# Kernel optimization log

Measured on AMD Instinct MI355X. Metric: run time of the kernel, lower is better.

## Reference

```python
import jax, jax.numpy as jnp
import numpy as np

N = 20000      # base graph nodes
S = 20         # nodes per subgraph
NC = N * S     # combined subgraph nodes = 400000
EC = 2_000_000 # combined subgraph edges
EB = 200_000   # base graph edges
NIN = 64
HOP = 16
D = NIN + HOP  # 80, conv width
NOUT = 64


def setup_inputs() -> dict:
    key = jax.random.key(0)
    ks = jax.random.split(key, 32)
    f32 = jnp.float32

    batch = jnp.repeat(jnp.arange(N), S)                      # subgraph id per combined node
    offs = jax.random.randint(ks[0], (NC,), 1, N)
    nodes_mapper = (batch + offs) % N                         # never equals batch
    cent_idx = jnp.arange(N) * S
    nodes_mapper = nodes_mapper.at[cent_idx].set(jnp.arange(N))  # exactly one centroid/subgraph

    edge_index = jax.random.randint(ks[1], (2, EC), 0, NC)
    edges_mapper = jax.random.randint(ks[2], (EC,), 0, EB)
    hop_indicator = jax.random.randint(ks[3], (NC,), 0, 19)   # +1 -> [1,19] < 20

    x = jax.random.normal(ks[4], (N, NIN), f32)
    edge_attr = jax.random.normal(ks[5], (EB, D), f32)

    def lin(k, i, o, s=0.05):
        return jax.random.normal(k, (i, o), f32) * s

    inp = dict(
        x=x, edge_attr=edge_attr,
        hop_table=jax.random.normal(ks[6], (20, HOP), f32) * 0.05,
        conv_w1=lin(ks[7], D, D), bn1_g=jnp.ones((D,), f32), bn1_b=jnp.zeros((D,), f32),
        conv_w2=lin(ks[8], D, D), bn2_g=jnp.ones((D,), f32), bn2_b=jnp.zeros((D,), f32),
        oe_w=lin(ks[9], D, NOUT), oe_b=jnp.zeros((NOUT,), f32),
        sub_w=lin(ks[10], NOUT, NOUT), sub_b=jnp.zeros((NOUT,), f32),
        sub_g=jnp.ones((NOUT,), f32), sub_bt=jnp.zeros((NOUT,), f32),
        ctx_w=lin(ks[11], NOUT, NOUT), ctx_b=jnp.zeros((NOUT,), f32),
        ctx_g=jnp.ones((NOUT,), f32), ctx_bt=jnp.zeros((NOUT,), f32),
        gc_w=lin(ks[12], HOP, NOUT), gc_b=jnp.zeros((NOUT,), f32),
        gs_w=lin(ks[13], HOP, NOUT), gs_b=jnp.zeros((NOUT,), f32),
        gx_w=lin(ks[14], HOP, NOUT), gx_b=jnp.zeros((NOUT,), f32),
        fo_w=lin(ks[15], NOUT, NOUT), fo_b=jnp.zeros((NOUT,), f32),
        fo_g=jnp.ones((NOUT,), f32), fo_bt=jnp.zeros((NOUT,), f32),
        nodes_mapper=nodes_mapper, edges_mapper=edges_mapper,
        edge_index=edge_index, batch=batch, hop_indicator=hop_indicator,
    )
    return inp


def reference(x, edge_attr, hop_table,
              conv_w1, bn1_g, bn1_b, conv_w2, bn2_g, bn2_b, oe_w, oe_b,
              sub_w, sub_b, sub_g, sub_bt, ctx_w, ctx_b, ctx_g, ctx_bt,
              gc_w, gc_b, gs_w, gs_b, gx_w, gx_b,
              fo_w, fo_b, fo_g, fo_bt,
              nodes_mapper, edges_mapper, edge_index, batch, hop_indicator):
    hop_emb = hop_table[hop_indicator + 1]                       # [NC, HOP]
    h = jnp.concatenate([x[nodes_mapper], hop_emb], axis=-1)     # [NC, D] gather + concat
    ea = edge_attr[edges_mapper]                                 # [EC, D] gather
    src, dst = edge_index[0], edge_index[1]

    def gine_layer(h, W, g, b):
        # GINEConv (eps=0, no bias): Linear(x_i + sum_j ReLU(x_j + e_ji)), then eval-BN + ReLU
        msg = jax.nn.relu(h[src] + ea)                           # [EC, D]
        agg = jax.ops.segment_sum(msg, dst, num_segments=NC)     # scatter-add
        out = (h + agg) @ W
        return jax.nn.relu(g * out + b)

    prev = h
    h = gine_layer(h, conv_w1, bn1_g, bn1_b) + prev
    prev = h
    h = gine_layer(h, conv_w2, bn2_g, bn2_b) + prev
    comb = h @ oe_w + oe_b                                       # [NC, NOUT] output encoder

    gate_c = jax.nn.sigmoid(hop_emb @ gc_w + gc_b)
    gate_s = jax.nn.sigmoid(hop_emb @ gs_w + gs_b)
    gate_x = jax.nn.sigmoid(hop_emb @ gx_w + gx_b)

    # centroid: exactly one node per subgraph with mapper==batch -> masked segment_sum picks it
    mask = (nodes_mapper == batch).astype(comb.dtype)[:, None]
    centroid = jax.ops.segment_sum(comb * gate_c * mask, batch, num_segments=N)

    sub = jax.nn.relu(sub_g * (comb @ sub_w + sub_b) + sub_bt) * gate_s
    ctx = jax.nn.relu(ctx_g * (comb @ ctx_w + ctx_b) + ctx_bt) * gate_x

    ones = jnp.ones((NC,), comb.dtype)
    cnt_b = jnp.clip(jax.ops.segment_sum(ones, batch, num_segments=N), 1.0)
    cnt_m = jnp.clip(jax.ops.segment_sum(ones, nodes_mapper, num_segments=N), 1.0)
    sub_pool = jax.ops.segment_sum(sub, batch, num_segments=N) / cnt_b[:, None]
    ctx_pool = jax.ops.segment_sum(ctx, nodes_mapper, num_segments=N) / cnt_m[:, None]

    out = centroid + sub_pool + ctx_pool                         # embs_combine_mode='add'
    return fo_g * (out @ fo_w + fo_b) + fo_bt                    # out_encoder: Linear + eval-BN
```

## Files before the change

kernel.cpp:

```cpp
#include <hip/hip_runtime.h>
#include <hip/hip_bf16.h>

#define N_    20000
#define S_    20
#define NC_   400000
#define EC_   2000000
#define EB_   200000
#define NIN_  64
#define HOP_  16
#define D_    80
#define NOUT_ 64
#define NB_   1563
#define NBN_  79

typedef __attribute__((ext_vector_type(8))) short bf16x8;
typedef __attribute__((ext_vector_type(4))) float f32x4;
union FragU { uint4 u; bf16x8 b; };

__device__ __forceinline__ float2 bf2f(unsigned u) {
    float2 r;
    r.x = __uint_as_float(u << 16);
    r.y = __uint_as_float(u & 0xffff0000u);
    return r;
}
__device__ __forceinline__ unsigned f2bf_rne(float f) {
    unsigned u = __float_as_uint(f);
    return (u + 0x7fffu + ((u >> 16) & 1u)) >> 16;
}
__device__ __forceinline__ unsigned pack2(float a, float b) {
    return f2bf_rne(a) | (f2bf_rne(b) << 16);
}
__device__ __forceinline__ unsigned addpk(unsigned a, unsigned b) {
    float2 fa = bf2f(a), fb = bf2f(b);
    return pack2(fa.x + fb.x, fa.y + fb.y);
}
__device__ __forceinline__ uint4 addpk4(uint4 A, uint4 B) {
    return make_uint4(addpk(A.x, B.x), addpk(A.y, B.y), addpk(A.z, B.z), addpk(A.w, B.w));
}

__device__ __forceinline__ int blockExclScan(int v, int tid, int* lds, int* total) {
    int lane = tid & 63;
    int w = tid >> 6;
    int x = v;
    #pragma unroll
    for (int off = 1; off < 64; off <<= 1) {
        int y = __shfl_up(x, off, 64);
        if (lane >= off) x += y;
    }
    if (lane == 63) lds[w] = x;
    __syncthreads();
    if (tid == 0) {
        int acc = 0;
        #pragma unroll
        for (int i = 0; i < 4; i++) { int t = lds[i]; lds[4 + i] = acc; acc += t; }
        lds[8] = acc;
    }
    __syncthreads();
    int res = x - v + lds[4 + w];
    *total = lds[8];
    return res;
}

__global__ __launch_bounds__(256) void k_degree(const int* __restrict__ eidx, int* __restrict__ deg) {
    int e = blockIdx.x * 256 + threadIdx.x;
    if (e >= EC_) return;
    atomicAdd(&deg[eidx[EC_ + e]], 1);
}

__global__ __launch_bounds__(256) void k_hist(const int* __restrict__ mapper, int* __restrict__ cnt) {
    int i = blockIdx.x * 256 + threadIdx.x;
    if (i >= NC_) return;
    atomicAdd(&cnt[mapper[i]], 1);
}

__global__ __launch_bounds__(256) void k_bsum(const int* __restrict__ deg, int* __restrict__ bsums, int n) {
    __shared__ int lds[9];
    int i = blockIdx.x * 256 + threadIdx.x;
    int v = (i < n) ? deg[i] : 0;
    int tot;
    blockExclScan(v, threadIdx.x, lds, &tot);
    if (threadIdx.x == 0) bsums[blockIdx.x] = tot;
}

__global__ __launch_bounds__(256) void k_scan_bsums(int* __restrict__ bsums, int nb) {
    __shared__ int lds[9];
    int carry = 0;
    for (int base = 0; base < nb; base += 256) {
        int i = base + threadIdx.x;
        int v = (i < nb) ? bsums[i] : 0;
        int tot;
        int ex = blockExclScan(v, threadIdx.x, lds, &tot);
        if (i < nb) bsums[i] = ex + carry;
        carry += tot;
        __syncthreads();
    }
}

__global__ __launch_bounds__(256) void k_scan_apply(
    int* __restrict__ cursor, int* __restrict__ start, const int* __restrict__ bsums,
    int n, int total)
{
    __shared__ int lds[9];
    int i = blockIdx.x * 256 + threadIdx.x;
    int v = (i < n) ? cursor[i] : 0;
    int tot;
    int ex = blockExclScan(v, threadIdx.x, lds, &tot);
    if (i < n) {
        int s = ex + bsums[blockIdx.x];
        start[i] = s;
        cursor[i] = s;
    }
    if (blockIdx.x == 0 && threadIdx.x == 0) start[n] = total;
}

__global__ __launch_bounds__(256) void k_fill(
    const int* __restrict__ eidx, const int* __restrict__ emap,
    const int* __restrict__ hop,
    int* __restrict__ cursor, int2* __restrict__ e2)
{
    int e = blockIdx.x * 256 + threadIdx.x;
    if (e >= EC_) return;
    int src = eidx[e];
    int dst = eidx[EC_ + e];
    int pk = emap[e] * 32 + (hop[src] + 1);
    int pos = atomicAdd(&cursor[dst], 1);
    e2[pos] = make_int2(src, pk);
}

__global__ __launch_bounds__(256) void k_fill_nodes(
    const int* __restrict__ mapper, int* __restrict__ cursor, int* __restrict__ nidx)
{
    int i = blockIdx.x * 256 + threadIdx.x;
    if (i >= NC_) return;
    int pos = atomicAdd(&cursor[mapper[i]], 1);
    nidx[pos] = i;
}

__global__ __launch_bounds__(256) void k_xb16(unsigned* __restrict__ xb, const float* __restrict__ x) {
    int idx = blockIdx.x * 256 + threadIdx.x;
    if (idx >= N_ * 32) return;
    int row = idx >> 5, p = idx & 31;
    float2 v = *(const float2*)(x + (size_t)row * 64 + 2 * p);
    xb[idx] = pack2(v.x, v.y);
}
__global__ __launch_bounds__(160) void k_htb16(unsigned* __restrict__ htb, const float* __restrict__ ht) {
    int idx = threadIdx.x;
    int row = idx >> 3, p = idx & 7;
    float2 v = *(const float2*)(ht + (size_t)row * 16 + 2 * p);
    htb[idx] = pack2(v.x, v.y);
}

__global__ __launch_bounds__(256) void k_ea16(
    unsigned* __restrict__ eab, const float* __restrict__ ea)
{
    int idx = blockIdx.x * 256 + threadIdx.x;
    if (idx >= EB_ * 40) return;
    int row = idx / 40, t = idx - row * 40;
    float2 v = *(const float2*)(ea + (size_t)row * 80 + 2 * t);
    eab[idx] = pack2(v.x, v.y);
}

__global__ __launch_bounds__(64) void k_gates(
    const float* __restrict__ ht,
    const float* __restrict__ gc_w, const float* __restrict__ gc_b,
    const float* __restrict__ gs_w, const float* __restrict__ gs_b,
    const float* __restrict__ gx_w, const float* __restrict__ gx_b,
    float* __restrict__ gall)
{
    int h = blockIdx.x;
    int d = threadIdx.x;
    const float* htr = ht + h * 16;
    float a = gc_b[d], b = gs_b[d], c = gx_b[d];
    #pragma unroll
    for (int k = 0; k < 16; k++) {
        float hk = htr[k];
        a += hk * gc_w[k * 64 + d];
        b += hk * gs_w[k * 64 + d];
        c += hk * gx_w[k * 64 + d];
    }
    gall[h * 64 + d]            = 1.f / (1.f + __expf(-a));
    gall[(20 + h) * 64 + d]     = 1.f / (1.f + __expf(-b));
    gall[(40 + h) * 64 + d]     = 1.f / (1.f + __expf(-c));
}

template<int L, bool EA16>
__global__ __launch_bounds__(320) void k_agg(
    const unsigned* __restrict__ hin, const unsigned* __restrict__ xb,
    const unsigned* __restrict__ htb, const int* __restrict__ mapper,
    const unsigned* __restrict__ eab, const float* __restrict__ eaf,
    const int* __restrict__ start, const int2* __restrict__ e2,
    unsigned* __restrict__ agg)
{
    int tid = threadIdx.x;
    int grp = tid / 40;
    int p = tid - grp * 40;
    int node = blockIdx.x * 8 + grp;
    float ax = 0.f, ay = 0.f;
    int e = start[node], s1 = start[node + 1];

    auto hload = [&](int src, int pk) -> float2 {
        if (L == 1) {
            if (p < 32) {
                int xs = mapper[src];
                return bf2f(xb[(size_t)xs * 32 + p]);
            } else {
                return bf2f(htb[(pk & 31) * 8 + (p - 32)]);
            }
        } else {
            return bf2f(hin[(size_t)src * 40 + p]);
        }
    };
    auto eload = [&](int pk) -> float2 {
        int em = pk >> 5;
        if (EA16) return bf2f(eab[(size_t)em * 40 + p]);
        else      return *(const float2*)(eaf + (size_t)em * 80 + 2 * p);
    };

    for (; e + 4 <= s1; e += 4) {
        int2 d0 = e2[e], d1 = e2[e + 1], d2 = e2[e + 2], d3 = e2[e + 3];
        float2 h0 = hload(d0.x, d0.y), h1 = hload(d1.x, d1.y);
        float2 h2 = hload(d2.x, d2.y), h3 = hload(d3.x, d3.y);
        float2 q0 = eload(d0.y), q1 = eload(d1.y), q2 = eload(d2.y), q3 = eload(d3.y);
        ax += fmaxf(h0.x + q0.x, 0.f) + fmaxf(h1.x + q1.x, 0.f)
            + fmaxf(h2.x + q2.x, 0.f) + fmaxf(h3.x + q3.x, 0.f);
        ay += fmaxf(h0.y + q0.y, 0.f) + fmaxf(h1.y + q1.y, 0.f)
            + fmaxf(h2.y + q2.y, 0.f) + fmaxf(h3.y + q3.y, 0.f);
    }
    for (; e < s1; e++) {
        int2 d0 = e2[e];
        float2 h0 = hload(d0.x, d0.y);
        float2 q0 = eload(d0.y);
        ax += fmaxf(h0.x + q0.x, 0.f);
        ay += fmaxf(h0.y + q0.y, 0.f);
    }
    agg[(size_t)node * 40 + p] = pack2(ax, ay);
}

template<int L>
__global__ __launch_bounds__(256) void k_lin(
    const unsigned* __restrict__ hbase, const unsigned* __restrict__ agg,
    unsigned* __restrict__ outp,
    const unsigned* __restrict__ xb, const unsigned* __restrict__ htb,
    const int* __restrict__ mapper, const int* __restrict__ hop,
    const float* __restrict__ W, const float* __restrict__ gv, const float* __restrict__ bv)
{
    __shared__ unsigned sWB[5 * 16 * 49];
    int tid = threadIdx.x;
    for (int i = tid; i < 5 * 16 * 49; i += 256) {
        int t = i / 784, r2 = i % 784, cc = r2 / 49, kp = r2 % 49;
        int col = 16 * t + cc;
        sWB[i] = (kp < 40) ? pack2(W[(2 * kp) * D_ + col], W[(2 * kp + 1) * D_ + col]) : 0u;
    }
    __syncthreads();

    int w = tid >> 6;
    int lane = tid & 63;
    int q = lane >> 4;
    int c = lane & 15;
    int base = (blockIdx.x * 4 + w) * 16;

    const unsigned* ar = agg + (size_t)(base + c) * 40;
    uint4 g0 = *(const uint4*)(ar + 4 * q);
    uint4 g1 = *(const uint4*)(ar + 16 + 4 * q);
    uint4 g2 = (q < 2) ? *(const uint4*)(ar + 32 + 4 * q) : make_uint4(0u, 0u, 0u, 0u);
    uint4 h0v, h1v, h2v;
    if (L == 1) {
        int m = mapper[base + c];
        int hp = hop[base + c] + 1;
        const unsigned* xr = xb + (size_t)m * 32;
        h0v = *(const uint4*)(xr + 4 * q);
        h1v = *(const uint4*)(xr + 16 + 4 * q);
        h2v = (q < 2) ? *(const uint4*)(htb + hp * 8 + 4 * q) : make_uint4(0u, 0u, 0u, 0u);
    } else {
        const unsigned* hr = hbase + (size_t)(base + c) * 40;
        h0v = *(const uint4*)(hr + 4 * q);
        h1v = *(const uint4*)(hr + 16 + 4 * q);
        h2v = (q < 2) ? *(const uint4*)(hr + 32 + 4 * q) : make_uint4(0u, 0u, 0u, 0u);
    }
    FragU a0, a1, a2;
    a0.u = addpk4(h0v, g0);
    a1.u = addpk4(h1v, g1);
    a2.u = (q < 2) ? addpk4(h2v, g2) : make_uint4(0u, 0u, 0u, 0u);

    f32x4 acc[5];
    #pragma unroll
    for (int t = 0; t < 5; t++) {
        const unsigned* pb = sWB + (t * 16 + c) * 49 + 4 * q;
        FragU b0, b1, b2;
        b0.u = *(const uint4*)(pb);
        b1.u = *(const uint4*)(pb + 16);
        b2.u = *(const uint4*)(pb + 32);
        f32x4 z = {0.f, 0.f, 0.f, 0.f};
        acc[t] = __builtin_amdgcn_mfma_f32_16x16x32_bf16(a0.b, b0.b, z, 0, 0, 0);
        acc[t] = __builtin_amdgcn_mfma_f32_16x16x32_bf16(a1.b, b1.b, acc[t], 0, 0, 0);
        acc[t] = __builtin_amdgcn_mfma_f32_16x16x32_bf16(a2.b, b2.b, acc[t], 0, 0, 0);
    }

    int mm2[4], hp2[4];
    if (L == 1) {
        #pragma unroll
        for (int r = 0; r < 4; r++) {
            int row = base + 4 * q + r;
            mm2[r] = mapper[row];
            hp2[r] = hop[row] + 1;
        }
    }
    #pragma unroll
    for (int t = 0; t < 5; t++) {
        int col = 16 * t + c;
        float gc_ = gv[col], bc_ = bv[col];
        #pragma unroll
        for (int r = 0; r < 4; r++) {
            int row = base + 4 * q + r;
            unsigned hu;
            if (L == 1) {
                hu = (t < 4) ? xb[(size_t)mm2[r] * 32 + 8 * t + (c >> 1)]
                             : htb[hp2[r] * 8 + (c >> 1)];
            } else {
                hu = hbase[(size_t)row * 40 + 8 * t + (c >> 1)];
            }
            float2 hf = bf2f(hu);
            float hres = (c & 1) ? hf.y : hf.x;
            float o = fmaxf(gc_ * acc[t][r] + bc_, 0.f) + hres;
            float partner = __shfl_xor(o, 1);
            if (!(c & 1)) outp[(size_t)row * 40 + 8 * t + (c >> 1)] = pack2(o, partner);
        }
    }
}

__global__ __launch_bounds__(256) void k_headm(
    const unsigned* __restrict__ h2u, const int* __restrict__ hop,
    const int* __restrict__ mapper, const float* __restrict__ gall,
    const float* __restrict__ oe_w, const float* __restrict__ oe_b,
    const float* __restrict__ sub_w, const float* __restrict__ sub_b,
    const float* __restrict__ sub_g, const float* __restrict__ sub_bt,
    const float* __restrict__ ctx_w, const float* __restrict__ ctx_b,
    const float* __restrict__ ctx_g, const float* __restrict__ ctx_bt,
    float* __restrict__ cent, float* __restrict__ subp, unsigned* __restrict__ ctxv)
{
    __shared__ unsigned sOE[4 * 16 * 48];
    __shared__ unsigned sSB[4 * 16 * 40];
    __shared__ unsigned sCX[4 * 16 * 40];
    __shared__ float    sT[4][16 * 68];
    int tid = threadIdx.x;
    for (int i = tid; i < 4 * 16 * 48; i += 256) {
        int t = i / (16 * 48), r2 = i % (16 * 48), cc = r2 / 48, kp = r2 % 48;
        int col = 16 * t + cc;
        sOE[i] = (kp < 40) ? pack2(oe_w[(2 * kp) * 64 + col], oe_w[(2 * kp + 1) * 64 + col]) : 0u;
    }
    for (int i = tid; i < 4 * 16 * 40; i += 256) {
        int t = i / (16 * 40), r2 = i % (16 * 40), cc = r2 / 40, kp = r2 % 40;
        int col = 16 * t + cc;
        bool ok = kp < 32;
        sSB[i] = ok ? pack2(sub_w[(2 * kp) * 64 + col], sub_w[(2 * kp + 1) * 64 + col]) : 0u;
        sCX[i] = ok ? pack2(ctx_w[(2 * kp) * 64 + col], ctx_w[(2 * kp + 1) * 64 + col]) : 0u;
    }
    __syncthreads();

    int w = tid >> 6;
    int lane = tid & 63;
    int q = lane >> 4;
    int c = lane & 15;
    int base = (blockIdx.x * 4 + w) * 16;

    const uint4* hrow = (const uint4*)(h2u + (size_t)(base + c) * 40);
    FragU a0, a1, a2;
    a0.u = hrow[q];
    a1.u = hrow[4 + q];
    a2.u = make_uint4(0u, 0u, 0u, 0u);
    if (q < 2) a2.u = hrow[8 + q];

    f32x4 acc[4];
    #pragma unroll
    for (int t = 0; t < 4; t++) {
        const unsigned* pb = sOE + (t * 16 + c) * 48 + 4 * q;
        FragU b0, b1, b2;
        b0.u = *(const uint4*)(pb);
        b1.u = *(const uint4*)(pb + 16);
        b2.u = *(const uint4*)(pb + 32);
        f32x4 z = {0.f, 0.f, 0.f, 0.f};
        acc[t] = __builtin_amdgcn_mfma_f32_16x16x32_bf16(a0.b, b0.b, z, 0, 0, 0);
        acc[t] = __builtin_amdgcn_mfma_f32_16x16x32_bf16(a1.b, b1.b, acc[t], 0, 0, 0);
        acc[t] = __builtin_amdgcn_mfma_f32_16x16x32_bf16(a2.b, b2.b, acc[t], 0, 0, 0);
    }

    int mm[4], hn[4];
    #pragma unroll
    for (int r = 0; r < 4; r++) {
        int node = base + 4 * q + r;
        mm[r] = mapper[node];
        hn[r] = hop[node] + 1;
    }
    int sgA = base / S_;
    int k0 = (sgA + 1) * S_ - base;
    if (k0 > 16) k0 = 16;

    #pragma unroll
    for (int t = 0; t < 4; t++) {
        int col = 16 * t + c;
        float ob = oe_b[col];
        #pragma unroll
        for (int r = 0; r < 4; r++) {
            int row = 4 * q + r;
            float v = acc[t][r] + ob;
            sT[w][row * 68 + col] = v;
            int sg = (row < k0) ? sgA : sgA + 1;
            if (mm[r] == sg) {
                cent[(size_t)sg * 64 + col] = v * gall[hn[r] * 64 + col];
            }
        }
    }

    const float* trp = &sT[w][c * 68 + 8 * q];
    float4 v0 = *(const float4*)(trp);
    float4 v1 = *(const float4*)(trp + 4);
    float4 v2 = *(const float4*)(trp + 32);
    float4 v3 = *(const float4*)(trp + 36);
    FragU ap0, ap1;
    ap0.u = make_uint4(pack2(v0.x, v0.y), pack2(v0.z, v0.w), pack2(v1.x, v1.y), pack2(v1.z, v1.w));
    ap1.u = make_uint4(pack2(v2.x, v2.y), pack2(v2.z, v2.w), pack2(v3.x, v3.y), pack2(v3.z, v3.w));

    f32x4 sa[4], ca[4];
    #pragma unroll
    for (int t = 0; t < 4; t++) {
        const unsigned* ps = sSB + (t * 16 + c) * 40 + 4 * q;
        const unsigned* pc = sCX + (t * 16 + c) * 40 + 4 * q;
        FragU b0, b1, d0, d1;
        b0.u = *(const uint4*)(ps);
        b1.u = *(const uint4*)(ps + 16);
        d0.u = *(const uint4*)(pc);
        d1.u = *(const uint4*)(pc + 16);
        f32x4 z = {0.f, 0.f, 0.f, 0.f};
        sa[t] = __builtin_amdgcn_mfma_f32_16x16x32_bf16(ap0.b, b0.b, z, 0, 0, 0);
        sa[t] = __builtin_amdgcn_mfma_f32_16x16x32_bf16(ap1.b, b1.b, sa[t], 0, 0, 0);
        ca[t] = __builtin_amdgcn_mfma_f32_16x16x32_bf16(ap0.b, d0.b, z, 0, 0, 0);
        ca[t] = __builtin_amdgcn_mfma_f32_16x16x32_bf16(ap1.b, d1.b, ca[t], 0, 0, 0);
    }

    #pragma unroll
    for (int t = 0; t < 4; t++) {
        int col = 16 * t + c;
        float sb = sub_b[col], sgm = sub_g[col], sbt = sub_bt[col];
        float cb = ctx_b[col], cgm = ctx_g[col], cbt = ctx_bt[col];
        float sA = 0.f, sB = 0.f;
        #pragma unroll
        for (int r = 0; r < 4; r++) {
            int row = 4 * q + r;
            float sval = fmaxf(sgm * (sa[t][r] + sb) + sbt, 0.f) * gall[(20 + hn[r]) * 64 + col];
            float cval = fmaxf(cgm * (ca[t][r] + cb) + cbt, 0.f) * gall[(40 + hn[r]) * 64 + col];
            float partner = __shfl_xor(cval, 1);
            if ((c & 1) == 0) {
                ctxv[(size_t)(base + row) * 32 + (col >> 1)] = pack2(cval, partner);
            }
            if (row < k0) sA += sval; else sB += sval;
        }
        sA += __shfl_xor(sA, 16); sA += __shfl_xor(sA, 32);
        sB += __shfl_xor(sB, 16); sB += __shfl_xor(sB, 32);
        if (q == 0) {
            atomicAdd(&subp[(size_t)sgA * 64 + col], sA);
            if (k0 < 16) atomicAdd(&subp[(size_t)(sgA + 1) * 64 + col], sB);
        }
    }
}

__global__ __launch_bounds__(256) void k_ctxpool(
    const unsigned* __restrict__ ctxv, const int* __restrict__ nstart,
    const int* __restrict__ nidx, float* __restrict__ ctxp)
{
    int w = threadIdx.x >> 6, d = threadIdx.x & 63;
    int n = blockIdx.x * 4 + w;
    if (n >= N_) return;
    int s0 = nstart[n], s1 = nstart[n + 1];
    int dh = d >> 1;
    float acc = 0.f;
    int i = s0;
    for (; i + 4 <= s1; i += 4) {
        int r0 = nidx[i], r1 = nidx[i + 1], r2 = nidx[i + 2], r3 = nidx[i + 3];
        float2 f0 = bf2f(ctxv[(size_t)r0 * 32 + dh]);
        float2 f1 = bf2f(ctxv[(size_t)r1 * 32 + dh]);
        float2 f2 = bf2f(ctxv[(size_t)r2 * 32 + dh]);
        float2 f3 = bf2f(ctxv[(size_t)r3 * 32 + dh]);
        acc += (d & 1) ? (f0.y + f1.y + f2.y + f3.y) : (f0.x + f1.x + f2.x + f3.x);
    }
    for (; i < s1; i++) {
        float2 f = bf2f(ctxv[(size_t)nidx[i] * 32 + dh]);
        acc += (d & 1) ? f.y : f.x;
    }
    ctxp[(size_t)n * 64 + d] = acc;
}

__global__ __launch_bounds__(256) void k_final(
    const float* __restrict__ cent, const float* __restrict__ subp, const float* __restrict__ ctxp,
    const int* __restrict__ nstart,
    const float* __restrict__ fo_w, const float* __restrict__ fo_b,
    const float* __restrict__ fo_g, const float* __restrict__ fo_bt,
    float* __restrict__ out)
{
    __shared__ float sW[64 * 64];
    int tid = threadIdx.x;
    for (int i = tid; i < 4096; i += 256) sW[i] = fo_w[i];
    int d = tid & 63, grp = tid >> 6;
    float rb = fo_b[d], rg = fo_g[d], rbt = fo_bt[d];
    __syncthreads();
    for (int n = blockIdx.x * 4 + grp; n < N_; n += gridDim.x * 4) {
        float cm = (float)max(nstart[n + 1] - nstart[n], 1);
        size_t o = (size_t)n * 64 + d;
        float r = cent[o] + subp[o] * (1.f / 20.f) + ctxp[o] / cm;
        float dot = rb;
        #pragma unroll 8
        for (int k = 0; k < 64; k++) dot += __shfl(r, k) * sW[k * 64 + d];
        out[o] = rg * dot + rbt;
    }
}

extern "C" void kernel_launch(void* const* d_in, const int* in_sizes, int n_in,
                              void* d_out, int out_size, void* d_ws, size_t ws_size,
                              hipStream_t stream) {
    const float* x         = (const float*)d_in[0];
    const float* edge_attr = (const float*)d_in[1];
    const float* hop_table = (const float*)d_in[2];
    const float* conv_w1   = (const float*)d_in[3];
    const float* bn1_g     = (const float*)d_in[4];
    const float* bn1_b     = (const float*)d_in[5];
    const float* conv_w2   = (const float*)d_in[6];
    const float* bn2_g     = (const float*)d_in[7];
    const float* bn2_b     = (const float*)d_in[8];
    const float* oe_w      = (const float*)d_in[9];
    const float* oe_b      = (const float*)d_in[10];
    const float* sub_w     = (const float*)d_in[11];
    const float* sub_b     = (const float*)d_in[12];
    const float* sub_g     = (const float*)d_in[13];
    const float* sub_bt    = (const float*)d_in[14];
    const float* ctx_w     = (const float*)d_in[15];
    const float* ctx_b     = (const float*)d_in[16];
    const float* ctx_g     = (const float*)d_in[17];
    const float* ctx_bt    = (const float*)d_in[18];
    const float* gc_w      = (const float*)d_in[19];
    const float* gc_b      = (const float*)d_in[20];
    const float* gs_w      = (const float*)d_in[21];
    const float* gs_b      = (const float*)d_in[22];
    const float* gx_w      = (const float*)d_in[23];
    const float* gx_b      = (const float*)d_in[24];
    const float* fo_w      = (const float*)d_in[25];
    const float* fo_b      = (const float*)d_in[26];
    const float* fo_g      = (const float*)d_in[27];
    const float* fo_bt     = (const float*)d_in[28];
    const int* nodes_mapper  = (const int*)d_in[29];
    const int* edges_mapper  = (const int*)d_in[30];
    const int* edge_index    = (const int*)d_in[31];
    const int* batch         = (const int*)d_in[32];
    const int* hop_indicator = (const int*)d_in[33];
    (void)batch;
    float* out = (float*)d_out;

    size_t off = 0;
    auto alloc = [&](size_t bytes) -> char* {
        char* p = (char*)d_ws + off;
        off = (off + bytes + 255) & ~(size_t)255;
        return p;
    };
    unsigned* hbuf0 = (unsigned*)alloc((size_t)NC_ * 40 * 4);
    unsigned* hbuf1 = (unsigned*)alloc((size_t)NC_ * 40 * 4);
    int*   start    = (int*)alloc((size_t)(NC_ + 1) * 4);
    int*   cursor   = (int*)alloc((size_t)NC_ * 4);
    int*   bsums    = (int*)alloc(2048 * 4);
    int2*  e2       = (int2*)alloc((size_t)EC_ * 8);
    float* cent     = (float*)alloc((size_t)N_ * 64 * 4);
    float* subp     = (float*)alloc((size_t)N_ * 64 * 4);
    float* ctxp     = (float*)alloc((size_t)N_ * 64 * 4);
    int*   nstart   = (int*)alloc((size_t)(N_ + 1) * 4);
    int*   cursor_n = (int*)alloc((size_t)N_ * 4);
    int*   bsums_n  = (int*)alloc(256 * 4);
    int*   nidx     = (int*)alloc((size_t)NC_ * 4);
    float* gall     = (float*)alloc((size_t)60 * 64 * 4);
    unsigned* xb    = (unsigned*)alloc((size_t)N_ * 32 * 4);
    unsigned* htb   = (unsigned*)alloc((size_t)20 * 8 * 4);
    size_t ea16_bytes = (size_t)EB_ * 40 * 4;
    bool use_ea16 = (off + ea16_bytes + 256) <= ws_size;
    unsigned* eab = use_ea16 ? (unsigned*)alloc(ea16_bytes) : nullptr;
    unsigned* ctxv = hbuf1;
    (void)in_sizes; (void)n_in; (void)out_size;

    hipMemsetAsync(cursor, 0, (size_t)NC_ * 4, stream);
    hipMemsetAsync(cursor_n, 0, (size_t)N_ * 4, stream);
    hipMemsetAsync(subp, 0, (size_t)N_ * 64 * 4, stream);

    k_xb16<<<(N_ * 32 + 255) / 256, 256, 0, stream>>>(xb, x);
    k_htb16<<<1, 160, 0, stream>>>(htb, hop_table);
    k_gates<<<20, 64, 0, stream>>>(hop_table, gc_w, gc_b, gs_w, gs_b, gx_w, gx_b, gall);
    if (use_ea16)
        k_ea16<<<(EB_ * 40 + 255) / 256, 256, 0, stream>>>(eab, edge_attr);

    k_degree<<<(EC_ + 255) / 256, 256, 0, stream>>>(edge_index, cursor);
    k_bsum<<<NB_, 256, 0, stream>>>(cursor, bsums, NC_);
    k_scan_bsums<<<1, 256, 0, stream>>>(bsums, NB_);
    k_scan_apply<<<NB_, 256, 0, stream>>>(cursor, start, bsums, NC_, EC_);
    k_fill<<<(EC_ + 255) / 256, 256, 0, stream>>>(edge_index, edges_mapper, hop_indicator,
                                                  cursor, e2);

    k_hist<<<(NC_ + 255) / 256, 256, 0, stream>>>(nodes_mapper, cursor_n);
    k_bsum<<<NBN_, 256, 0, stream>>>(cursor_n, bsums_n, N_);
    k_scan_bsums<<<1, 256, 0, stream>>>(bsums_n, NBN_);
    k_scan_apply<<<NBN_, 256, 0, stream>>>(cursor_n, nstart, bsums_n, N_, NC_);
    k_fill_nodes<<<(NC_ + 255) / 256, 256, 0, stream>>>(nodes_mapper, cursor_n, nidx);

    if (use_ea16)
        k_agg<1, true><<<NC_ / 8, 320, 0, stream>>>(nullptr, xb, htb, nodes_mapper,
                                                    eab, edge_attr, start, e2, hbuf0);
    else
        k_agg<1, false><<<NC_ / 8, 320, 0, stream>>>(nullptr, xb, htb, nodes_mapper,
                                                     eab, edge_attr, start, e2, hbuf0);
    k_lin<1><<<NC_ / 64, 256, 0, stream>>>(nullptr, hbuf0, hbuf1, xb, htb,
                                           nodes_mapper, hop_indicator,
                                           conv_w1, bn1_g, bn1_b);

    if (use_ea16)
        k_agg<2, true><<<NC_ / 8, 320, 0, stream>>>(hbuf1, xb, htb, nodes_mapper,
                                                    eab, edge_attr, start, e2, hbuf0);
    else
        k_agg<2, false><<<NC_ / 8, 320, 0, stream>>>(hbuf1, xb, htb, nodes_mapper,
                                                     eab, edge_attr, start, e2, hbuf0);
    k_lin<2><<<NC_ / 64, 256, 0, stream>>>(hbuf1, hbuf0, hbuf0, xb, htb,
                                           nodes_mapper, hop_indicator,
                                           conv_w2, bn2_g, bn2_b);

    k_headm<<<NC_ / 64, 256, 0, stream>>>(hbuf0, hop_indicator, nodes_mapper, gall,
                                          oe_w, oe_b, sub_w, sub_b, sub_g, sub_bt,
                                          ctx_w, ctx_b, ctx_g, ctx_bt,
                                          cent, subp, ctxv);

    k_ctxpool<<<N_ / 4, 256, 0, stream>>>(ctxv, nstart, nidx, ctxp);

    k_final<<<1280, 256, 0, stream>>>(cent, subp, ctxp, nstart, fo_w, fo_b, fo_g, fo_bt, out);
}
```

Measured before the change: 1.202 ms.

## Fuse GINE edge aggregation into the MFMA linear kernel

Merges the separate aggregation kernel and the linear/BN kernel into one kernel per conv layer. Each lane gathers neighbour and edge-attribute rows directly in the MFMA fragment layout (uint4 chunks), accumulates in fp32 registers, and feeds the sum straight into the MFMA. This removes the intermediate agg buffer write/read and one launch per layer. In exchange, each 16-lane group walks its own node's edge list under a wave-wide __any loop, so waves wait on the highest-degree node and may lose load balance and latency hiding compared to the 40-thread-per-node layout.

```diff
diff --git a/kernel.cpp b/kernel.cpp
--- a/kernel.cpp
+++ b/kernel.cpp
@@ -30,12 +30,27 @@
 __device__ __forceinline__ unsigned pack2(float a, float b) {
     return f2bf_rne(a) | (f2bf_rne(b) << 16);
 }
-__device__ __forceinline__ unsigned addpk(unsigned a, unsigned b) {
-    float2 fa = bf2f(a), fb = bf2f(b);
-    return pack2(fa.x + fb.x, fa.y + fb.y);
-}
-__device__ __forceinline__ uint4 addpk4(uint4 A, uint4 B) {
-    return make_uint4(addpk(A.x, B.x), addpk(A.y, B.y), addpk(A.z, B.z), addpk(A.w, B.w));
+
+__device__ __forceinline__ void acc4(float* A, uint4 hv, uint4 ev) {
+    const unsigned* hp = (const unsigned*)&hv;
+    const unsigned* ep = (const unsigned*)&ev;
+    #pragma unroll
+    for (int j = 0; j < 4; j++) {
+        float2 hs = bf2f(hp[j]);
+        float2 eq = bf2f(ep[j]);
+        A[2 * j]     += fmaxf(hs.x + eq.x, 0.f);
+        A[2 * j + 1] += fmaxf(hs.y + eq.y, 0.f);
+    }
+}
+__device__ __forceinline__ void acc4f(float* A, uint4 hv, const float* er, int off) {
+    const unsigned* hp = (const unsigned*)&hv;
+    #pragma unroll
+    for (int j = 0; j < 4; j++) {
+        float2 hs = bf2f(hp[j]);
+        float2 eq = *(const float2*)(er + 2 * (off + j));
+        A[2 * j]     += fmaxf(hs.x + eq.x, 0.f);
+        A[2 * j + 1] += fmaxf(hs.y + eq.y, 0.f);
+    }
 }
 
 __device__ __forceinline__ int blockExclScan(int v, int tid, int* lds, int* total) {
@@ -184,64 +199,13 @@
 }
 
 template<int L, bool EA16>
-__global__ __launch_bounds__(320) void k_agg(
-    const unsigned* __restrict__ hin, const unsigned* __restrict__ xb,
-    const unsigned* __restrict__ htb, const int* __restrict__ mapper,
+__global__ __launch_bounds__(256) void k_gine_f(
+    const unsigned* __restrict__ hin,
+    const unsigned* __restrict__ xb, const unsigned* __restrict__ htb,
+    const int* __restrict__ mapper, const int* __restrict__ hop,
     const unsigned* __restrict__ eab, const float* __restrict__ eaf,
     const int* __restrict__ start, const int2* __restrict__ e2,
-    unsigned* __restrict__ agg)
-{
-    int tid = threadIdx.x;
-    int grp = tid / 40;
-    int p = tid - grp * 40;
-    int node = blockIdx.x * 8 + grp;
-    float ax = 0.f, ay = 0.f;
-    int e = start[node], s1 = start[node + 1];
-
-    auto hload = [&](int src, int pk) -> float2 {
-        if (L == 1) {
-            if (p < 32) {
-                int xs = mapper[src];
-                return bf2f(xb[(size_t)xs * 32 + p]);
-            } else {
-                return bf2f(htb[(pk & 31) * 8 + (p - 32)]);
-            }
-        } else {
-            return bf2f(hin[(size_t)src * 40 + p]);
-        }
-    };
-    auto eload = [&](int pk) -> float2 {
-        int em = pk >> 5;
-        if (EA16) return bf2f(eab[(size_t)em * 40 + p]);
-        else      return *(const float2*)(eaf + (size_t)em * 80 + 2 * p);
-    };
-
-    for (; e + 4 <= s1; e += 4) {
-        int2 d0 = e2[e], d1 = e2[e + 1], d2 = e2[e + 2], d3 = e2[e + 3];
-        float2 h0 = hload(d0.x, d0.y), h1 = hload(d1.x, d1.y);
-        float2 h2 = hload(d2.x, d2.y), h3 = hload(d3.x, d3.y);
-        float2 q0 = eload(d0.y), q1 = eload(d1.y), q2 = eload(d2.y), q3 = eload(d3.y);
-        ax += fmaxf(h0.x + q0.x, 0.f) + fmaxf(h1.x + q1.x, 0.f)
-            + fmaxf(h2.x + q2.x, 0.f) + fmaxf(h3.x + q3.x, 0.f);
-        ay += fmaxf(h0.y + q0.y, 0.f) + fmaxf(h1.y + q1.y, 0.f)
-            + fmaxf(h2.y + q2.y, 0.f) + fmaxf(h3.y + q3.y, 0.f);
-    }
-    for (; e < s1; e++) {
-        int2 d0 = e2[e];
-        float2 h0 = hload(d0.x, d0.y);
-        float2 q0 = eload(d0.y);
-        ax += fmaxf(h0.x + q0.x, 0.f);
-        ay += fmaxf(h0.y + q0.y, 0.f);
-    }
-    agg[(size_t)node * 40 + p] = pack2(ax, ay);
-}
-
-template<int L>
-__global__ __launch_bounds__(256) void k_lin(
-    const unsigned* __restrict__ hbase, const unsigned* __restrict__ agg,
     unsigned* __restrict__ outp,
-    const unsigned* __restrict__ xb, const unsigned* __restrict__ htb,
-    const int* __restrict__ mapper, const int* __restrict__ hop,
     const float* __restrict__ W, const float* __restrict__ gv, const float* __restrict__ bv)
 {
     __shared__ unsigned sWB[5 * 16 * 49];
@@ -258,29 +222,100 @@
     int q = lane >> 4;
     int c = lane & 15;
     int base = (blockIdx.x * 4 + w) * 16;
-
-    const unsigned* ar = agg + (size_t)(base + c) * 40;
-    uint4 g0 = *(const uint4*)(ar + 4 * q);
-    uint4 g1 = *(const uint4*)(ar + 16 + 4 * q);
-    uint4 g2 = (q < 2) ? *(const uint4*)(ar + 32 + 4 * q) : make_uint4(0u, 0u, 0u, 0u);
+    int node = base + c;
+    int off0 = 4 * q, off1 = 16 + 4 * q, off2 = 32 + 4 * q;
+
+    float A0[8] = {0.f, 0.f, 0.f, 0.f, 0.f, 0.f, 0.f, 0.f};
+    float A1[8] = {0.f, 0.f, 0.f, 0.f, 0.f, 0.f, 0.f, 0.f};
+    float A2[8] = {0.f, 0.f, 0.f, 0.f, 0.f, 0.f, 0.f, 0.f};
+    uint4 zz = make_uint4(0u, 0u, 0u, 0u);
+
+    int e = start[node];
+    int s1 = start[node + 1];
+    while (__any(e < s1)) {
+        bool a0 = e < s1;
+        bool a1 = (e + 1) < s1;
+        int ee0 = max(min(e, s1 - 1), 0);
+        int ee1 = max(min(e + 1, s1 - 1), 0);
+        int2 ed0 = e2[ee0];
+        int2 ed1 = e2[ee1];
+        uint4 s00, s01, s02, s10, s11, s12;
+        if (L == 1) {
+            int m0 = mapper[ed0.x];
+            int m1 = mapper[ed1.x];
+            const unsigned* x0 = xb + (size_t)m0 * 32;
+            const unsigned* x1 = xb + (size_t)m1 * 32;
+            s00 = *(const uint4*)(x0 + off0);
+            s01 = *(const uint4*)(x0 + off1);
+            s02 = (q < 2) ? *(const uint4*)(htb + (ed0.y & 31) * 8 + off0) : zz;
+            s10 = *(const uint4*)(x1 + off0);
+            s11 = *(const uint4*)(x1 + off1);
+            s12 = (q < 2) ? *(const uint4*)(htb + (ed1.y & 31) * 8 + off0) : zz;
+        } else {
+            const unsigned* h0 = hin + (size_t)ed0.x * 40;
+            const unsigned* h1 = hin + (size_t)ed1.x * 40;
+            s00 = *(const uint4*)(h0 + off0);
+            s01 = *(const uint4*)(h0 + off1);
+            s02 = (q < 2) ? *(const uint4*)(h0 + off2) : zz;
+            s10 = *(const uint4*)(h1 + off0);
+            s11 = *(const uint4*)(h1 + off1);
+            s12 = (q < 2) ? *(const uint4*)(h1 + off2) : zz;
+        }
+        int em0 = ed0.y >> 5, em1 = ed1.y >> 5;
+        if (EA16) {
+            const unsigned* e0p = eab + (size_t)em0 * 40;
+            const unsigned* e1p = eab + (size_t)em1 * 40;
+            uint4 q00 = *(const uint4*)(e0p + off0);
+            uint4 q01 = *(const uint4*)(e0p + off1);
+            uint4 q02 = (q < 2) ? *(const uint4*)(e0p + off2) : zz;
+            uint4 q10 = *(const uint4*)(e1p + off0);
+            uint4 q11 = *(const uint4*)(e1p + off1);
+            uint4 q12 = (q < 2) ? *(const uint4*)(e1p + off2) : zz;
+            if (a0) { acc4(A0, s00, q00); acc4(A1, s01, q01); if (q < 2) acc4(A2, s02, q02); }
+            if (a1) { acc4(A0, s10, q10); acc4(A1, s11, q11); if (q < 2) acc4(A2, s12, q12); }
+        } else {
+            const float* e0p = eaf + (size_t)em0 * 80;
+            const float* e1p = eaf + (size_t)em1 * 80;
+            if (a0) { acc4f(A0, s00, e0p, off0); acc4f(A1, s01, e0p, off1); if (q < 2) acc4f(A2, s02, e0p, off2); }
+            if (a1) { acc4f(A0, s10, e1p, off0); acc4f(A1, s11, e1p, off1); if (q < 2) acc4f(A2, s12, e1p, off2); }
+        }
+        e += 2;
+    }
+
     uint4 h0v, h1v, h2v;
     if (L == 1) {
-        int m = mapper[base + c];
-        int hp = hop[base + c] + 1;
+        int m = mapper[node];
+        int hp = hop[node] + 1;
         const unsigned* xr = xb + (size_t)m * 32;
-        h0v = *(const uint4*)(xr + 4 * q);
-        h1v = *(const uint4*)(xr + 16 + 4 * q);
-        h2v = (q < 2) ? *(const uint4*)(htb + hp * 8 + 4 * q) : make_uint4(0u, 0u, 0u, 0u);
+        h0v = *(const uint4*)(xr + off0);
+        h1v = *(const uint4*)(xr + off1);
+        h2v = (q < 2) ? *(const uint4*)(htb + hp * 8 + off0) : zz;
     } else {
-        const unsigned* hr = hbase + (size_t)(base + c) * 40;
-        h0v = *(const uint4*)(hr + 4 * q);
-        h1v = *(const uint4*)(hr + 16 + 4 * q);
-        h2v = (q < 2) ? *(const uint4*)(hr + 32 + 4 * q) : make_uint4(0u, 0u, 0u, 0u);
-    }
-    FragU a0, a1, a2;
-    a0.u = addpk4(h0v, g0);
-    a1.u = addpk4(h1v, g1);
-    a2.u = (q < 2) ? addpk4(h2v, g2) : make_uint4(0u, 0u, 0u, 0u);
+        const unsigned* hr = hin + (size_t)node * 40;
+        h0v = *(const uint4*)(hr + off0);
+        h1v = *(const uint4*)(hr + off1);
+        h2v = (q < 2) ? *(const uint4*)(hr + off2) : zz;
+    }
+
+    FragU a0F, a1F, a2F;
+    {
+        const unsigned* hp0 = (const unsigned*)&h0v;
+        const unsigned* hp1 = (const unsigned*)&h1v;
+        const unsigned* hp2 = (const unsigned*)&h2v;
+        unsigned r0[4], r1[4], r2[4];
+        #pragma unroll
+        for (int j = 0; j < 4; j++) {
+            float2 f0 = bf2f(hp0[j]);
+            float2 f1 = bf2f(hp1[j]);
+            float2 f2 = bf2f(hp2[j]);
+            r0[j] = pack2(A0[2 * j] + f0.x, A0[2 * j + 1] + f0.y);
+            r1[j] = pack2(A1[2 * j] + f1.x, A1[2 * j + 1] + f1.y);
+            r2[j] = (q < 2) ? pack2(A2[2 * j] + f2.x, A2[2 * j + 1] + f2.y) : 0u;
+        }
+        a0F.u = make_uint4(r0[0], r0[1], r0[2], r0[3]);
+        a1F.u = make_uint4(r1[0], r1[1], r1[2], r1[3]);
+        a2F.u = make_uint4(r2[0], r2[1], r2[2], r2[3]);
+    }
 
     f32x4 acc[5];
     #pragma unroll
@@ -291,18 +326,18 @@
         b1.u = *(const uint4*)(pb + 16);
         b2.u = *(const uint4*)(pb + 32);
         f32x4 z = {0.f, 0.f, 0.f, 0.f};
-        acc[t] = __builtin_amdgcn_mfma_f32_16x16x32_bf16(a0.b, b0.b, z, 0, 0, 0);
-        acc[t] = __builtin_amdgcn_mfma_f32_16x16x32_bf16(a1.b, b1.b, acc[t], 0, 0, 0);
-        acc[t] = __builtin_amdgcn_mfma_f32_16x16x32_bf16(a2.b, b2.b, acc[t], 0, 0, 0);
-    }
-
-    int mm2[4], hp2[4];
+        acc[t] = __builtin_amdgcn_mfma_f32_16x16x32_bf16(a0F.b, b0.b, z, 0, 0, 0);
+        acc[t] = __builtin_amdgcn_mfma_f32_16x16x32_bf16(a1F.b, b1.b, acc[t], 0, 0, 0);
+        acc[t] = __builtin_amdgcn_mfma_f32_16x16x32_bf16(a2F.b, b2.b, acc[t], 0, 0, 0);
+    }
+
+    int mm2[4], hp2v[4];
     if (L == 1) {
         #pragma unroll
         for (int r = 0; r < 4; r++) {
             int row = base + 4 * q + r;
             mm2[r] = mapper[row];
-            hp2[r] = hop[row] + 1;
+            hp2v[r] = hop[row] + 1;
         }
     }
     #pragma unroll
@@ -315,9 +350,9 @@
             unsigned hu;
             if (L == 1) {
                 hu = (t < 4) ? xb[(size_t)mm2[r] * 32 + 8 * t + (c >> 1)]
-                             : htb[hp2[r] * 8 + (c >> 1)];
+                             : htb[hp2v[r] * 8 + (c >> 1)];
             } else {
-                hu = hbase[(size_t)row * 40 + 8 * t + (c >> 1)];
+                hu = hin[(size_t)row * 40 + 8 * t + (c >> 1)];
             }
             float2 hf = bf2f(hu);
             float hres = (c & 1) ? hf.y : hf.x;
@@ -604,25 +639,21 @@
     k_scan_apply<<<NBN_, 256, 0, stream>>>(cursor_n, nstart, bsums_n, N_, NC_);
     k_fill_nodes<<<(NC_ + 255) / 256, 256, 0, stream>>>(nodes_mapper, cursor_n, nidx);
 
-    if (use_ea16)
-        k_agg<1, true><<<NC_ / 8, 320, 0, stream>>>(nullptr, xb, htb, nodes_mapper,
-                                                    eab, edge_attr, start, e2, hbuf0);
-    else
-        k_agg<1, false><<<NC_ / 8, 320, 0, stream>>>(nullptr, xb, htb, nodes_mapper,
-                                                     eab, edge_attr, start, e2, hbuf0);
-    k_lin<1><<<NC_ / 64, 256, 0, stream>>>(nullptr, hbuf0, hbuf1, xb, htb,
-                                           nodes_mapper, hop_indicator,
-                                           conv_w1, bn1_g, bn1_b);
-
-    if (use_ea16)
-        k_agg<2, true><<<NC_ / 8, 320, 0, stream>>>(hbuf1, xb, htb, nodes_mapper,
-                                                    eab, edge_attr, start, e2, hbuf0);
-    else
-        k_agg<2, false><<<NC_ / 8, 320, 0, stream>>>(hbuf1, xb, htb, nodes_mapper,
-                                                     eab, edge_attr, start, e2, hbuf0);
-    k_lin<2><<<NC_ / 64, 256, 0, stream>>>(hbuf1, hbuf0, hbuf0, xb, htb,
-                                           nodes_mapper, hop_indicator,
-                                           conv_w2, bn2_g, bn2_b);
+    if (use_ea16) {
+        k_gine_f<1, true><<<NC_ / 64, 256, 0, stream>>>(nullptr, xb, htb, nodes_mapper,
+                                                        hop_indicator, eab, edge_attr,
+                                                        start, e2, hbuf1, conv_w1, bn1_g, bn1_b);
+        k_gine_f<2, true><<<NC_ / 64, 256, 0, stream>>>(hbuf1, xb, htb, nodes_mapper,
+                                                        hop_indicator, eab, edge_attr,
+                                                        start, e2, hbuf0, conv_w2, bn2_g, bn2_b);
+    } else {
+        k_gine_f<1, false><<<NC_ / 64, 256, 0, stream>>>(nullptr, xb, htb, nodes_mapper,
+                                                         hop_indicator, eab, edge_attr,
+                                                         start, e2, hbuf1, conv_w1, bn1_g, bn1_b);
+        k_gine_f<2, false><<<NC_ / 64, 256, 0, stream>>>(hbuf1, xb, htb, nodes_mapper,
+                                                         hop_indicator, eab, edge_attr,
+                                                         start, e2, hbuf0, conv_w2, bn2_g, bn2_b);
+    }
 
     k_headm<<<NC_ / 64, 256, 0, stream>>>(hbuf0, hop_indicator, nodes_mapper, gall,
                                           oe_w, oe_b, sub_w, sub_b, sub_g, sub_bt,
```

Result: faster. 1.118 ms (-7.0%).
